# Kernel tuning notes

Measured on AMD Instinct MI355X. Metric: run time of the kernel, lower is better.

Reference implementation:

```python
import jax, jax.numpy as jnp
import numpy as np

IN_FEATURES = 212445
NODE_SIZES = [IN_FEATURES, 65536, 16384, 128]
N_CLASSES = 20
BATCH = 32


def setup_inputs() -> dict:
    key = jax.random.key(0)
    ks = jax.random.split(key, 16)
    inp = {
        "x": jax.random.normal(ks[0], (BATCH, IN_FEATURES), dtype=jnp.float32),
        "W0": jax.random.normal(ks[1], (32, 1), dtype=jnp.float32) * 0.1,
        "b0": jax.random.normal(ks[2], (32,), dtype=jnp.float32) * 0.1,
        "W1": jax.random.normal(ks[3], (64, 32), dtype=jnp.float32) * 0.1,
        "b1": jax.random.normal(ks[4], (64,), dtype=jnp.float32) * 0.1,
        "W2": jax.random.normal(ks[5], (128, 64), dtype=jnp.float32) * 0.1,
        "b2": jax.random.normal(ks[6], (128,), dtype=jnp.float32) * 0.1,
        "fc_w": jax.random.normal(ks[7], (N_CLASSES, 128 * 128), dtype=jnp.float32) * 0.01,
        "fc_b": jax.random.normal(ks[8], (N_CLASSES,), dtype=jnp.float32) * 0.01,
        # random-tree adjacency: each input node has one parent output node
        "parent0": jax.random.randint(ks[9], (NODE_SIZES[0],), 0, NODE_SIZES[1], dtype=jnp.int32),
        "parent1": jax.random.randint(ks[10], (NODE_SIZES[1],), 0, NODE_SIZES[2], dtype=jnp.int32),
        "parent2": jax.random.randint(ks[11], (NODE_SIZES[2],), 0, NODE_SIZES[3], dtype=jnp.int32),
    }
    return inp


def _fgl(z, parent, n_out, W, b):
    """FGL layer: tree-adjacency reduction over nodes + channel mix.
    z: [N, C_in, n_in] -> [N, C_out, n_out]
    """
    N, C, n_in = z.shape
    # segment-sum reduce input nodes into their parent output node
    zt = jnp.moveaxis(z, 2, 0).reshape(n_in, N * C)          # [n_in, N*C]
    s = jax.ops.segment_sum(zt, parent, num_segments=n_out)  # [n_out, N*C]
    s = jnp.moveaxis(s.reshape(n_out, N, C), 0, 2)           # [N, C_in, n_out]
    # channel mixing (weight-normed linear over channels, shared across nodes)
    return jnp.einsum("oc,ncj->noj", W, s) + b[None, :, None]


def reference(x, W0, b0, W1, b1, W2, b2, fc_w, fc_b, parent0, parent1, parent2):
    N = x.shape[0]
    z = x[:, None, :]                                   # [N, 1, in_features]
    z = _fgl(z, parent0, NODE_SIZES[1], W0, b0)         # [N, 32, 65536]
    z = _fgl(z, parent1, NODE_SIZES[2], W1, b1)         # [N, 64, 16384]
    z = _fgl(z, parent2, NODE_SIZES[3], W2, b2)         # [N, 128, 128]
    logits = z.reshape(N, -1) @ fc_w.T + fc_b           # [N, n_classes]
    return logits
```

## Files before the change

### kernel.cpp

```cpp
#include <hip/hip_runtime.h>

#define IN_FEATURES 212445
#define N1 65536
#define N2 16384
#define NCLS 20
#define BATCH 32
#define HIST_BLOCKS 32
#define MCHUNK 1024
#define MBLOCKS ((IN_FEATURES + MCHUNK - 1) / MCHUNK)
#define TOTF (BATCH * IN_FEATURES)
#define TOTF4 (TOTF / 4)
#define CF4 2048
#define NT3B ((TOTF4 + CF4 - 1) / CF4)


__global__ __launch_bounds__(256) void k_setup(
    const float* __restrict__ W0, const float* __restrict__ b0,
    const float* __restrict__ W1, const float* __restrict__ b1,
    const float* __restrict__ W2, const float* __restrict__ b2,
    const float* __restrict__ fc_w,
    const int* __restrict__ p0, const int* __restrict__ p1,
    const int* __restrict__ p2,
    float* __restrict__ t3, int* __restrict__ hist,
    float* __restrict__ Sa, float* __restrict__ Sv,
    float* __restrict__ Sw, float* __restrict__ Sb,
    int* __restrict__ midx)
{
    int t = threadIdx.x;
    int b = blockIdx.x;
    if (b == 0) {
        for (int s = t; s < BATCH * 128; s += 256) t3[s] = 0.f;
    } else if (b < 1 + NCLS) {
        int cls = b - 1;
        __shared__ float su1[64], sv1[64];
        __shared__ float lu[128], lv[128], lw[128], lb[128];
        __shared__ float qA[256], qV[256], qW[256], qB[256];
        if (t < 64) {
            float a = 0.f, bb = 0.f;
            for (int c = 0; c < 32; ++c) {
                float w = W1[t * 32 + c];
                a  += w * W0[c];
                bb += w * b0[c];
            }
            su1[t] = a; sv1[t] = bb;
        }
        __syncthreads();
        if (t < 128) {
            float a = 0.f, bb = 0.f, cc = 0.f;
            for (int j = 0; j < 64; ++j) {
                float w = W2[t * 64 + j];
                a  += w * su1[j];
                bb += w * sv1[j];
                cc += w * b1[j];
            }
            lu[t] = a; lv[t] = bb; lw[t] = cc; lb[t] = b2[t];
        }
        __syncthreads();
        int m = t & 127, h = t >> 7;
        const float* fw = fc_w + cls * 16384 + m;
        float A = 0.f, V = 0.f, Wt = 0.f, Bt = 0.f;
        #pragma unroll 16
        for (int o = h * 64; o < h * 64 + 64; ++o) {
            float wv = fw[o * 128];
            A  += wv * lu[o];
            V  += wv * lv[o];
            Wt += wv * lw[o];
            Bt += wv * lb[o];
        }
        qA[t] = A; qV[t] = V; qW[t] = Wt; qB[t] = Bt;
        __syncthreads();
        if (h == 0) {
            Sa[cls * 128 + m] = qA[m] + qA[128 + m];
            Sv[cls * 128 + m] = qV[m] + qV[128 + m];
            Sw[cls * 128 + m] = qW[m] + qW[128 + m];
            Sb[cls * 128 + m] = qB[m] + qB[128 + m];
        }
    } else if (b < 1 + NCLS + HIST_BLOCKS) {
        __shared__ int hA[128], hB[128];
        if (t < 128) { hA[t] = 0; hB[t] = 0; }
        __syncthreads();
        const int total = N1 + N2;
        const int stride = HIST_BLOCKS * 256;
        int hb = b - (1 + NCLS);
        for (int idx = hb * 256 + t; idx < total; idx += stride) {
            if (idx < N1) atomicAdd(&hA[p2[p1[idx]]], 1);
            else          atomicAdd(&hB[p2[idx - N1]], 1);
        }
        __syncthreads();
        hist[hb * 256 + t] = (t < 128) ? hA[t] : hB[t - 128];
    } else {
        int mb = b - (1 + NCLS + HIST_BLOCKS);
        int base = mb * MCHUNK;
        #pragma unroll
        for (int u = 0; u < MCHUNK / 256; ++u) {
            int i = base + u * 256 + t;
            if (i < IN_FEATURES) midx[i] = p2[p1[p0[i]]];
        }
    }
}

__global__ __launch_bounds__(256) void k_t3(
    const float* __restrict__ x, const int* __restrict__ midx,
    float* __restrict__ t3)
{
    __shared__ float hist[4 * 256];
    int t = threadIdx.x;
    #pragma unroll
    for (int s = t; s < 1024; s += 256) hist[s] = 0.f;
    __syncthreads();

    int b = blockIdx.x;
    int f0 = b * (CF4 * 4);
    int row0 = f0 / IN_FEATURES;
    int rb = row0 * IN_FEATURES;
    float* hw = hist + (t >> 6) * 256;
    const float4* x4 = (const float4*)x;
    int base4 = b * CF4 + t;

    if (b != NT3B - 1) {
        for (int kk = 0; kk < 4; ++kk) {
            int fA = base4 + (2 * kk) * 256;
            int fB = base4 + (2 * kk + 1) * 256;
            float4 vA = x4[fA];
            float4 vB = x4[fB];
            int lA = fA * 4 - rb;
            int lB = fB * 4 - rb;
            int mi[8], sl[8];
            #pragma unroll
            for (int e = 0; e < 4; ++e) {
                int l = lA + e; int sg = (l >= IN_FEATURES);
                sl[e] = sg; mi[e] = midx[sg ? l - IN_FEATURES : l];
            }
            #pragma unroll
            for (int e = 0; e < 4; ++e) {
                int l = lB + e; int sg = (l >= IN_FEATURES);
                sl[4 + e] = sg; mi[4 + e] = midx[sg ? l - IN_FEATURES : l];
            }
            atomicAdd(&hw[sl[0] * 128 + mi[0]], vA.x);
            atomicAdd(&hw[sl[1] * 128 + mi[1]], vA.y);
            atomicAdd(&hw[sl[2] * 128 + mi[2]], vA.z);
            atomicAdd(&hw[sl[3] * 128 + mi[3]], vA.w);
            atomicAdd(&hw[sl[4] * 128 + mi[4]], vB.x);
            atomicAdd(&hw[sl[5] * 128 + mi[5]], vB.y);
            atomicAdd(&hw[sl[6] * 128 + mi[6]], vB.z);
            atomicAdd(&hw[sl[7] * 128 + mi[7]], vB.w);
        }
    } else {
        for (int kk = 0; kk < 8; ++kk) {
            int f4 = base4 + kk * 256;
            if (f4 < TOTF4) {
                float4 v = x4[f4];
                int l0 = f4 * 4 - rb;
                float vv[4] = {v.x, v.y, v.z, v.w};
                #pragma unroll
                for (int e = 0; e < 4; ++e) {
                    int l = l0 + e; int sg = (l >= IN_FEATURES);
                    atomicAdd(&hw[sg * 128 + midx[sg ? l - IN_FEATURES : l]], vv[e]);
                }
            }
        }
    }
    __syncthreads();
    if (t < 128) {
        float s0 = hist[t] + hist[256 + t] + hist[512 + t] + hist[768 + t];
        atomicAdd(&t3[row0 * 128 + t], s0);
        int bnd = rb + IN_FEATURES;
        int fend = f0 + CF4 * 4; if (fend > TOTF) fend = TOTF;
        if (row0 + 1 < BATCH && bnd < fend) {
            float s1 = hist[128 + t] + hist[384 + t] + hist[640 + t] + hist[896 + t];
            atomicAdd(&t3[(row0 + 1) * 128 + t], s1);
        }
    }
}

__global__ __launch_bounds__(256) void k_final(
    const float* __restrict__ fc_b,
    const float* __restrict__ Sa, const float* __restrict__ Sv,
    const float* __restrict__ Sw, const float* __restrict__ Sb,
    const int* __restrict__ hist, const float* __restrict__ t3,
    float* __restrict__ out)
{
    __shared__ float sA[128], red[128], r2[256];
    __shared__ float st3[BATCH * 129];
    __shared__ float sconst;
    int t = threadIdx.x;
    int cls = blockIdx.x;

    if (t < 128) {
        int c2 = 0, cn2 = 0;
        #pragma unroll
        for (int hb = 0; hb < HIST_BLOCKS; ++hb) {
            c2  += hist[hb * 256 + t];
            cn2 += hist[hb * 256 + 128 + t];
        }
        sA[t]  = Sa[cls * 128 + t];
        red[t] = (float)c2 * Sv[cls * 128 + t]
               + (float)cn2 * Sw[cls * 128 + t]
               + Sb[cls * 128 + t];
    }
    for (int s = t; s < BATCH * 128; s += 256)
        st3[(s >> 7) * 129 + (s & 127)] = t3[s];
    __syncthreads();
    for (int s2 = 64; s2 > 0; s2 >>= 1) {
        if (t < s2) red[t] += red[t + s2];
        __syncthreads();
    }
    if (t == 0) sconst = red[0] + fc_b[cls];
    __syncthreads();

    int n = t >> 3, oc = t & 7;
    const float* tr = st3 + n * 129 + oc * 16;
    const float* ar = sA + oc * 16;
    float s = 0.f;
    #pragma unroll
    for (int k = 0; k < 16; ++k) s += ar[k] * tr[k];
    r2[t] = s;
    __syncthreads();
    if (oc == 0) {
        float tot = sconst;
        #pragma unroll
        for (int k = 0; k < 8; ++k) tot += r2[t + k];
        out[n * NCLS + cls] = tot;
    }
}

extern "C" void kernel_launch(void* const* d_in, const int* in_sizes, int n_in,
                              void* d_out, int out_size, void* d_ws, size_t ws_size,
                              hipStream_t stream)
{
    const float* x    = (const float*)d_in[0];
    const float* W0   = (const float*)d_in[1];
    const float* b0   = (const float*)d_in[2];
    const float* W1   = (const float*)d_in[3];
    const float* b1   = (const float*)d_in[4];
    const float* W2   = (const float*)d_in[5];
    const float* b2   = (const float*)d_in[6];
    const float* fc_w = (const float*)d_in[7];
    const float* fc_b = (const float*)d_in[8];
    const int*   p0   = (const int*)d_in[9];
    const int*   p1   = (const int*)d_in[10];
    const int*   p2   = (const int*)d_in[11];

    char* ws = (char*)d_ws;
    float* t3   = (float*)(ws + 0);
    int*   hist = (int*)(ws + 16384);
    float* Sa   = (float*)(ws + 49152);
    float* Sv   = (float*)(ws + 59392);
    float* Sw   = (float*)(ws + 69632);
    float* Sb   = (float*)(ws + 79872);
    int*   midx = (int*)(ws + 90112);

    k_setup<<<1 + NCLS + HIST_BLOCKS + MBLOCKS, 256, 0, stream>>>(
        W0, b0, W1, b1, W2, b2, fc_w, p0, p1, p2, t3, hist, Sa, Sv, Sw, Sb, midx);
    k_t3<<<NT3B, 256, 0, stream>>>(x, midx, t3);
    k_final<<<NCLS, 256, 0, stream>>>(fc_b, Sa, Sv, Sw, Sb, hist, t3,
                                      (float*)d_out);
}
```

Before: 139.8 us.

## Replace shared-memory atomic histogram with per-thread private LDS bins

The x-reduction kernel drops shared-memory atomicAdd into four replicated histograms. Each of 128 threads now owns a private column of a 128x128 LDS histogram and does plain read-modify-write adds, then each thread sums one bin across all threads. Blocks cover 16K elements and fast-path chunks that do not cross a row boundary, with a segmented fallback for the rest. The aim is to remove LDS atomic contention and serialization, at the cost of 64KB of LDS per block, which limits occupancy, and fewer threads per block.

New measurement: 141.4 us. About the same (+1.1%).

```diff
diff --git a/kernel.cpp b/kernel.cpp
--- a/kernel.cpp
+++ b/kernel.cpp
@@ -9,9 +9,8 @@
 #define MCHUNK 1024
 #define MBLOCKS ((IN_FEATURES + MCHUNK - 1) / MCHUNK)
 #define TOTF (BATCH * IN_FEATURES)
-#define TOTF4 (TOTF / 4)
-#define CF4 2048
-#define NT3B ((TOTF4 + CF4 - 1) / CF4)
+#define EPB 16384
+#define NT3B ((TOTF + EPB - 1) / EPB)
 
 
 __global__ __launch_bounds__(256) void k_setup(
@@ -99,76 +98,83 @@
     }
 }
 
-__global__ __launch_bounds__(256) void k_t3(
+__global__ __launch_bounds__(128) void k_t3(
     const float* __restrict__ x, const int* __restrict__ midx,
     float* __restrict__ t3)
 {
-    __shared__ float hist[4 * 256];
+    __shared__ __align__(16) float hist[128 * 128];
     int t = threadIdx.x;
+    float4 z4 = make_float4(0.f, 0.f, 0.f, 0.f);
+    float4* hz = (float4*)hist;
     #pragma unroll
-    for (int s = t; s < 1024; s += 256) hist[s] = 0.f;
+    for (int s = t; s < 4096; s += 128) hz[s] = z4;
     __syncthreads();
 
     int b = blockIdx.x;
-    int f0 = b * (CF4 * 4);
-    int row0 = f0 / IN_FEATURES;
-    int rb = row0 * IN_FEATURES;
-    float* hw = hist + (t >> 6) * 256;
+    int f0 = b * EPB;
+    int fend = f0 + EPB; if (fend > TOTF) fend = TOTF;
+    int row = f0 / IN_FEATURES;
+    int rowbase = row * IN_FEATURES;
+    int bnd = rowbase + IN_FEATURES;
     const float4* x4 = (const float4*)x;
-    int base4 = b * CF4 + t;
-
-    if (b != NT3B - 1) {
-        for (int kk = 0; kk < 4; ++kk) {
-            int fA = base4 + (2 * kk) * 256;
-            int fB = base4 + (2 * kk + 1) * 256;
-            float4 vA = x4[fA];
-            float4 vB = x4[fB];
-            int lA = fA * 4 - rb;
-            int lB = fB * 4 - rb;
-            int mi[8], sl[8];
+
+    if (fend == f0 + EPB && fend <= bnd) {
+        int i0 = f0 >> 2;
+        #pragma unroll 2
+        for (int k = 0; k < 16; ++k) {
+            int ia = i0 + k * 256 + t;
+            int ib = ia + 128;
+            float4 va = x4[ia];
+            float4 vb = x4[ib];
+            int la = ia * 4 - rowbase;
+            int lb = ib * 4 - rowbase;
+            int m0 = midx[la],     m1 = midx[la + 1];
+            int m2 = midx[la + 2], m3 = midx[la + 3];
+            int m4 = midx[lb],     m5 = midx[lb + 1];
+            int m6 = midx[lb + 2], m7 = midx[lb + 3];
+            hist[m0 * 128 + t] += va.x;
+            hist[m1 * 128 + t] += va.y;
+            hist[m2 * 128 + t] += va.z;
+            hist[m3 * 128 + t] += va.w;
+            hist[m4 * 128 + t] += vb.x;
+            hist[m5 * 128 + t] += vb.y;
+            hist[m6 * 128 + t] += vb.z;
+            hist[m7 * 128 + t] += vb.w;
+        }
+        __syncthreads();
+        const float4* hr = (const float4*)(hist + t * 128);
+        float s = 0.f;
+        #pragma unroll
+        for (int j = 0; j < 32; ++j) {
+            float4 hv = hr[(j + t) & 31];
+            s += hv.x + hv.y + hv.z + hv.w;
+        }
+        atomicAdd(&t3[row * 128 + t], s);
+    } else {
+        int f = f0;
+        for (;;) {
+            int segEnd = fend < bnd ? fend : bnd;
+            for (int g = f + t; g < segEnd; g += 128) {
+                float v = x[g];
+                int m = midx[g - rowbase];
+                hist[m * 128 + t] += v;
+            }
+            __syncthreads();
+            const float4* hr = (const float4*)(hist + t * 128);
+            float s = 0.f;
             #pragma unroll
-            for (int e = 0; e < 4; ++e) {
-                int l = lA + e; int sg = (l >= IN_FEATURES);
-                sl[e] = sg; mi[e] = midx[sg ? l - IN_FEATURES : l];
-            }
+            for (int j = 0; j < 32; ++j) {
+                float4 hv = hr[(j + t) & 31];
+                s += hv.x + hv.y + hv.z + hv.w;
+            }
+            atomicAdd(&t3[row * 128 + t], s);
+            f = segEnd;
+            if (f >= fend) break;
+            __syncthreads();
             #pragma unroll
-            for (int e = 0; e < 4; ++e) {
-                int l = lB + e; int sg = (l >= IN_FEATURES);
-                sl[4 + e] = sg; mi[4 + e] = midx[sg ? l - IN_FEATURES : l];
-            }
-            atomicAdd(&hw[sl[0] * 128 + mi[0]], vA.x);
-            atomicAdd(&hw[sl[1] * 128 + mi[1]], vA.y);
-            atomicAdd(&hw[sl[2] * 128 + mi[2]], vA.z);
-            atomicAdd(&hw[sl[3] * 128 + mi[3]], vA.w);
-            atomicAdd(&hw[sl[4] * 128 + mi[4]], vB.x);
-            atomicAdd(&hw[sl[5] * 128 + mi[5]], vB.y);
-            atomicAdd(&hw[sl[6] * 128 + mi[6]], vB.z);
-            atomicAdd(&hw[sl[7] * 128 + mi[7]], vB.w);
-        }
-    } else {
-        for (int kk = 0; kk < 8; ++kk) {
-            int f4 = base4 + kk * 256;
-            if (f4 < TOTF4) {
-                float4 v = x4[f4];
-                int l0 = f4 * 4 - rb;
-                float vv[4] = {v.x, v.y, v.z, v.w};
-                #pragma unroll
-                for (int e = 0; e < 4; ++e) {
-                    int l = l0 + e; int sg = (l >= IN_FEATURES);
-                    atomicAdd(&hw[sg * 128 + midx[sg ? l - IN_FEATURES : l]], vv[e]);
-                }
-            }
-        }
-    }
-    __syncthreads();
-    if (t < 128) {
-        float s0 = hist[t] + hist[256 + t] + hist[512 + t] + hist[768 + t];
-        atomicAdd(&t3[row0 * 128 + t], s0);
-        int bnd = rb + IN_FEATURES;
-        int fend = f0 + CF4 * 4; if (fend > TOTF) fend = TOTF;
-        if (row0 + 1 < BATCH && bnd < fend) {
-            float s1 = hist[128 + t] + hist[384 + t] + hist[640 + t] + hist[896 + t];
-            atomicAdd(&t3[(row0 + 1) * 128 + t], s1);
+            for (int s2 = t; s2 < 4096; s2 += 128) hz[s2] = z4;
+            __syncthreads();
+            row++; rowbase = bnd; bnd += IN_FEATURES;
         }
     }
 }
@@ -252,7 +258,7 @@
 
     k_setup<<<1 + NCLS + HIST_BLOCKS + MBLOCKS, 256, 0, stream>>>(
         W0, b0, W1, b1, W2, b2, fc_w, p0, p1, p2, t3, hist, Sa, Sv, Sw, Sb, midx);
-    k_t3<<<NT3B, 256, 0, stream>>>(x, midx, t3);
+    k_t3<<<NT3B, 128, 0, stream>>>(x, midx, t3);
     k_final<<<NCLS, 256, 0, stream>>>(fc_b, Sa, Sv, Sw, Sb, hist, t3,
                                       (float*)d_out);
 }
```
